# Performance work log

Measured on AMD Instinct MI355X. Metric: run time of the kernel, lower is better.

## Reference

```python
import jax, jax.numpy as jnp
import numpy as np

B, F, D = 32768, 2668, 64

def _xn(key, shape):
    # xavier_normal_: std = sqrt(2/(fan_in+fan_out))
    std = np.sqrt(2.0 / (shape[0] + shape[1]))
    return jax.random.normal(key, shape, dtype=jnp.float32) * std

def setup_inputs() -> dict:
    key = jax.random.key(0)
    ks = jax.random.split(key, 16)
    fv = jax.random.uniform(ks[0], (B, F), dtype=jnp.float32)
    sizes = [(1, 'age_user_w'), (1, 'age_item_w'), (2, 'gender_user_w'), (2, 'gender_item_w'),
             (21, 'occupation_user_w'), (21, 'occupation_item_w'), (19, 'movie_user_w'), (19, 'movie_item_w'),
             (943, 'userid_user_w'), (943, 'userid_item_w'), (1682, 'itemid_user_w'), (1682, 'itemid_item_w')]
    inp = {'feature_vector': fv}
    for i, (n, name) in enumerate(sizes):
        inp[name] = _xn(ks[i + 1], (n, D))
    # nn.Linear(F,1): kaiming-uniform weight, uniform bias; plain uniform scale suffices for a reference
    bound = 1.0 / np.sqrt(F)
    inp['lin_w'] = jax.random.uniform(ks[13], (1, F), dtype=jnp.float32, minval=-bound, maxval=bound)
    inp['lin_b'] = jax.random.uniform(ks[14], (1,), dtype=jnp.float32, minval=-bound, maxval=bound)
    return inp

def reference(feature_vector, age_user_w, age_item_w, gender_user_w, gender_item_w,
              occupation_user_w, occupation_item_w, movie_user_w, movie_item_w,
              userid_user_w, userid_item_w, itemid_user_w, itemid_item_w, lin_w, lin_b):
    fv = feature_vector
    au = fv[:, 2626:2627] @ age_user_w          # [B, D] (note: column 2626 reused, as in source)
    ai = fv[:, 2626:2627] @ age_item_w
    gu = fv[:, 2626:2628] @ gender_user_w
    gi = fv[:, 2626:2628] @ gender_item_w
    ou = fv[:, 2628:2649] @ occupation_user_w
    oi = fv[:, 2628:2649] @ occupation_item_w
    mu = fv[:, 2649:2668] @ movie_user_w
    mi = fv[:, 2649:2668] @ movie_item_w
    uu = fv[:, 0:943] @ userid_user_w
    ui = fv[:, 0:943] @ userid_item_w
    tu = fv[:, 943:2625] @ itemid_user_w
    ti = fv[:, 943:2625] @ itemid_item_w
    cross = jnp.sum(au * gu + au * ou + ai * mu + au * uu + ai * tu
                    + gu * ou + gi * mu + gu * uu + gi * tu
                    + oi * mu + ou * uu + oi * tu
                    + mu * ui + mi * ti + ui * tu, axis=1)   # [B]
    logits = fv @ lin_w.T + lin_b + cross[:, None]           # [B, 1]
    return jax.nn.sigmoid(logits)
```

## Files before the change

kernel.cpp:

```cpp
#include <hip/hip_runtime.h>

#define FDIM 2668

typedef float f32x4 __attribute__((ext_vector_type(4)));
typedef _Float16 f16x8 __attribute__((ext_vector_type(8)));

#define G1_NK 30
#define G2_NK 53
#define G3_NK 2
#define G1_NT 9
#define G2_NT 9
#define G3_NT 29
#define BUF_BYTES (G3_NT * 1024)

#define HU 0
#define HT (G1_NK * G1_NT * 512)
#define HS (HT + G2_NK * G2_NT * 512)
#define H_TOTAL (HS + G3_NK * G3_NT * 512)

__global__ __launch_bounds__(256) void ffm_prep(
    const float* __restrict__ au_, const float* __restrict__ ai_,
    const float* __restrict__ gu_, const float* __restrict__ gi_,
    const float* __restrict__ ou_, const float* __restrict__ oi_,
    const float* __restrict__ mu_, const float* __restrict__ mi_,
    const float* __restrict__ uu_, const float* __restrict__ ui_,
    const float* __restrict__ tu_, const float* __restrict__ ti_,
    const float* __restrict__ lw, _Float16* __restrict__ ws) {
  int e = blockIdx.x * 256 + threadIdx.x;
  if (e >= H_TOTAL) return;
  float val = 0.f;
  int rel, ntiles;
  if (e < HT) { rel = e; ntiles = G1_NT; }
  else if (e < HS) { rel = e - HT; ntiles = G2_NT; }
  else { rel = e - HS; ntiles = G3_NT; }
  int perk = ntiles * 512;
  int kb = rel / perk;
  int r = rel - kb * perk;
  int nt = r >> 9; r &= 511;
  int lane = r >> 3, j = r & 7;
  int k = kb * 32 + ((lane >> 4) << 3) + j;
  int n = (nt << 4) + (lane & 15);

  if (e < HT) {
    if (k < 943) {
      if (n < 64) val = uu_[k * 64 + n];
      else if (n < 128) val = ui_[k * 64 + n - 64];
      else if (n == 128) val = lw[k];
    }
  } else if (e < HS) {
    int col = 940 + k;
    if (n < 64) { if (col >= 943 && col < 2625) val = tu_[(col - 943) * 64 + n]; }
    else if (n < 128) { if (col >= 943 && col < 2625) val = ti_[(col - 943) * 64 + n - 64]; }
    else if (n == 128) { if (col >= 943 && col <= 2635) val = lw[col]; }
  } else {
    int col = 2624 + k;
    if (n == 448) { if (col >= 2636 && col < 2668) val = lw[col]; }
    else if (n < 448) {
      int blk = n >> 6, d = n & 63;
      float ageu = (col == 2626) ? au_[d] : 0.f;
      float agei = (col == 2626) ? ai_[d] : 0.f;
      float genu = (col >= 2626 && col < 2628) ? gu_[(col - 2626) * 64 + d] : 0.f;
      float geni = (col >= 2626 && col < 2628) ? gi_[(col - 2626) * 64 + d] : 0.f;
      float occu = (col >= 2628 && col < 2649) ? ou_[(col - 2628) * 64 + d] : 0.f;
      float occi = (col >= 2628 && col < 2649) ? oi_[(col - 2628) * 64 + d] : 0.f;
      float movu = (col >= 2649 && col < 2668) ? mu_[(col - 2649) * 64 + d] : 0.f;
      float movi = (col >= 2649 && col < 2668) ? mi_[(col - 2649) * 64 + d] : 0.f;
      switch (blk) {
        case 0: val = ageu + genu + occu; break;
        case 1: val = agei + geni + occi; break;
        case 2: val = movu; break;
        case 3: val = movi; break;
        case 4: val = ageu; break;
        case 5: val = genu; break;
        case 6: val = occu; break;
      }
    }
  }
  ws[e] = (_Float16)val;
}

template <int NT>
__device__ __forceinline__ void stageB(const _Float16* __restrict__ src, char* lds,
                                       int bufOff, int tid, int wave) {
  constexpr int chunks = NT * 64;
#pragma unroll
  for (int base = 0; base < chunks; base += 256) {
    int idx = base + tid;
    if (idx < chunks) {
      __builtin_amdgcn_global_load_lds(
          (const __attribute__((address_space(1))) void*)(src + (size_t)idx * 8),
          (__attribute__((address_space(3))) void*)(lds + bufOff + (base + wave * 64) * 16),
          16, 0, 0);
    }
  }
}

template <bool GUARD>
__device__ __forceinline__ void loadA(f32x4& a0, f32x4& a1,
                                      const float* __restrict__ myrow, int c0) {
  f32x4 z = {0.f, 0.f, 0.f, 0.f};
  if (!GUARD || (c0 + 4) <= FDIM) a0 = *(const f32x4*)(myrow + c0); else a0 = z;
  if (!GUARD || (c0 + 8) <= FDIM) a1 = *(const f32x4*)(myrow + c0 + 4); else a1 = z;
}

template <int NT, bool GUARD>
__device__ __forceinline__ void gemm_phase(const float* __restrict__ myrow, int colbase,
                                           int nk, const _Float16* __restrict__ wsrc,
                                           char* lds, int tid, int lane, int kg, int wave,
                                           f32x4* acc) {
  stageB<NT>(wsrc, lds, 0, tid, wave);
  f32x4 a0, a1;
  loadA<GUARD>(a0, a1, myrow, colbase + kg * 8);
  int cur = 0;
  for (int kb = 0; kb < nk; ++kb) {
    __syncthreads();
    f32x4 n0 = {0.f, 0.f, 0.f, 0.f}, n1 = {0.f, 0.f, 0.f, 0.f};
    if (kb + 1 < nk) {
      stageB<NT>(wsrc + (size_t)(kb + 1) * (NT * 512), lds, (cur ^ 1) * BUF_BYTES, tid, wave);
      loadA<GUARD>(n0, n1, myrow, colbase + (kb + 1) * 32 + kg * 8);
    }
    f16x8 af;
#pragma unroll
    for (int i = 0; i < 4; ++i) { af[i] = (_Float16)a0[i]; af[4 + i] = (_Float16)a1[i]; }
    const char* buf = lds + cur * BUF_BYTES + lane * 16;
#pragma unroll
    for (int nt = 0; nt < NT; ++nt) {
      f16x8 bf = *(const f16x8*)(buf + nt * 1024);
      acc[nt] = __builtin_amdgcn_mfma_f32_16x16x32_f16(af, bf, acc[nt], 0, 0, 0);
    }
    a0 = n0; a1 = n1;
    cur ^= 1;
  }
}

__global__ __launch_bounds__(256, 2) void ffm_main(
    const float* __restrict__ fv, const _Float16* __restrict__ wp,
    const float* __restrict__ linb, float* __restrict__ out) {
  __shared__ __align__(16) char lds[2 * BUF_BYTES];
  const int tid = threadIdx.x;
  const int lane = tid & 63;
  const int wave = tid >> 6;
  const int nl = lane & 15;
  const int kg = lane >> 4;
  const int rowbase = blockIdx.x * 64 + wave * 16;
  const float* myrow = fv + (size_t)(rowbase + nl) * FDIM;
  const f32x4 zero4 = {0.f, 0.f, 0.f, 0.f};

  f32x4 s[G3_NT];
#pragma unroll
  for (int i = 0; i < G3_NT; ++i) s[i] = zero4;
  gemm_phase<G3_NT, true>(myrow, 2624, G3_NK, wp + HS, lds, tid, lane, kg, wave, s);

  f32x4 P[4], Q[4], MU[4], MI[4];
  f32x4 cross = s[28];
#pragma unroll
  for (int t = 0; t < 4; ++t) {
    P[t] = s[t]; Q[t] = s[4 + t]; MU[t] = s[8 + t]; MI[t] = s[12 + t];
    cross += s[16 + t] * (s[20 + t] + s[24 + t]) + s[20 + t] * s[24 + t] + MU[t] * Q[t];
  }

  f32x4 u[G1_NT];
#pragma unroll
  for (int i = 0; i < G1_NT; ++i) u[i] = zero4;
  gemm_phase<G1_NT, false>(myrow, 0, G1_NK, wp + HU, lds, tid, lane, kg, wave, u);
  cross += u[8];
#pragma unroll
  for (int t = 0; t < 4; ++t) {
    cross += u[t] * P[t] + u[4 + t] * MU[t];
    Q[t] += u[4 + t];
  }

  f32x4 v[G2_NT];
#pragma unroll
  for (int i = 0; i < G2_NT; ++i) v[i] = zero4;
  gemm_phase<G2_NT, false>(myrow, 940, G2_NK, wp + HT, lds, tid, lane, kg, wave, v);
  cross += v[8];
#pragma unroll
  for (int t = 0; t < 4; ++t) {
    cross += v[t] * Q[t] + v[4 + t] * MI[t];
  }

  float c0 = cross[0], c1 = cross[1], c2 = cross[2], c3 = cross[3];
#pragma unroll
  for (int m = 1; m <= 8; m <<= 1) {
    c0 += __shfl_xor(c0, m, 64);
    c1 += __shfl_xor(c1, m, 64);
    c2 += __shfl_xor(c2, m, 64);
    c3 += __shfl_xor(c3, m, 64);
  }
  if (nl == 0) {
    float lb = linb[0];
    int r = rowbase + kg * 4;
    out[r + 0] = 1.f / (1.f + __expf(-(c0 + lb)));
    out[r + 1] = 1.f / (1.f + __expf(-(c1 + lb)));
    out[r + 2] = 1.f / (1.f + __expf(-(c2 + lb)));
    out[r + 3] = 1.f / (1.f + __expf(-(c3 + lb)));
  }
}

extern "C" void kernel_launch(void* const* d_in, const int* in_sizes, int n_in,
                              void* d_out, int out_size, void* d_ws, size_t ws_size,
                              hipStream_t stream) {
  const float* fv    = (const float*)d_in[0];
  const float* age_u = (const float*)d_in[1];
  const float* age_i = (const float*)d_in[2];
  const float* gen_u = (const float*)d_in[3];
  const float* gen_i = (const float*)d_in[4];
  const float* occ_u = (const float*)d_in[5];
  const float* occ_i = (const float*)d_in[6];
  const float* mov_u = (const float*)d_in[7];
  const float* mov_i = (const float*)d_in[8];
  const float* uid_u = (const float*)d_in[9];
  const float* uid_i = (const float*)d_in[10];
  const float* iid_u = (const float*)d_in[11];
  const float* iid_i = (const float*)d_in[12];
  const float* lin_w = (const float*)d_in[13];
  const float* lin_b = (const float*)d_in[14];
  _Float16* ws = (_Float16*)d_ws;
  float* out = (float*)d_out;

  ffm_prep<<<(H_TOTAL + 255) / 256, 256, 0, stream>>>(
      age_u, age_i, gen_u, gen_i, occ_u, occ_i, mov_u, mov_i,
      uid_u, uid_i, iid_u, iid_i, lin_w, ws);
  ffm_main<<<32768 / 64, 256, 0, stream>>>(fv, ws, lin_b, out);
}
```

Baseline: 505.0 us.

## Load packed B fragments directly from global memory, dropping LDS staging and barriers

```diff
diff --git a/kernel.cpp b/kernel.cpp
--- a/kernel.cpp
+++ b/kernel.cpp
@@ -4,6 +4,7 @@
 
 typedef float f32x4 __attribute__((ext_vector_type(4)));
 typedef _Float16 f16x8 __attribute__((ext_vector_type(8)));
+typedef __fp16 fp16x2 __attribute__((ext_vector_type(2)));
 
 #define G1_NK 30
 #define G2_NK 53
@@ -11,7 +12,6 @@
 #define G1_NT 9
 #define G2_NT 9
 #define G3_NT 29
-#define BUF_BYTES (G3_NT * 1024)
 
 #define HU 0
 #define HT (G1_NK * G1_NT * 512)
@@ -79,22 +79,6 @@
   ws[e] = (_Float16)val;
 }
 
-template <int NT>
-__device__ __forceinline__ void stageB(const _Float16* __restrict__ src, char* lds,
-                                       int bufOff, int tid, int wave) {
-  constexpr int chunks = NT * 64;
-#pragma unroll
-  for (int base = 0; base < chunks; base += 256) {
-    int idx = base + tid;
-    if (idx < chunks) {
-      __builtin_amdgcn_global_load_lds(
-          (const __attribute__((address_space(1))) void*)(src + (size_t)idx * 8),
-          (__attribute__((address_space(3))) void*)(lds + bufOff + (base + wave * 64) * 16),
-          16, 0, 0);
-    }
-  }
-}
-
 template <bool GUARD>
 __device__ __forceinline__ void loadA(f32x4& a0, f32x4& a1,
                                       const float* __restrict__ myrow, int c0) {
@@ -103,40 +87,38 @@
   if (!GUARD || (c0 + 8) <= FDIM) a1 = *(const f32x4*)(myrow + c0 + 4); else a1 = z;
 }
 
+__device__ __forceinline__ f16x8 cvtA(const f32x4& a0, const f32x4& a1) {
+  union { f16x8 v; fp16x2 h[4]; } u;
+  u.h[0] = __builtin_amdgcn_cvt_pkrtz(a0[0], a0[1]);
+  u.h[1] = __builtin_amdgcn_cvt_pkrtz(a0[2], a0[3]);
+  u.h[2] = __builtin_amdgcn_cvt_pkrtz(a1[0], a1[1]);
+  u.h[3] = __builtin_amdgcn_cvt_pkrtz(a1[2], a1[3]);
+  return u.v;
+}
+
 template <int NT, bool GUARD>
 __device__ __forceinline__ void gemm_phase(const float* __restrict__ myrow, int colbase,
                                            int nk, const _Float16* __restrict__ wsrc,
-                                           char* lds, int tid, int lane, int kg, int wave,
-                                           f32x4* acc) {
-  stageB<NT>(wsrc, lds, 0, tid, wave);
+                                           int lane, int kg, f32x4* acc) {
+  const _Float16* bptr = wsrc + (size_t)lane * 8;
   f32x4 a0, a1;
   loadA<GUARD>(a0, a1, myrow, colbase + kg * 8);
-  int cur = 0;
   for (int kb = 0; kb < nk; ++kb) {
-    __syncthreads();
     f32x4 n0 = {0.f, 0.f, 0.f, 0.f}, n1 = {0.f, 0.f, 0.f, 0.f};
-    if (kb + 1 < nk) {
-      stageB<NT>(wsrc + (size_t)(kb + 1) * (NT * 512), lds, (cur ^ 1) * BUF_BYTES, tid, wave);
-      loadA<GUARD>(n0, n1, myrow, colbase + (kb + 1) * 32 + kg * 8);
-    }
-    f16x8 af;
-#pragma unroll
-    for (int i = 0; i < 4; ++i) { af[i] = (_Float16)a0[i]; af[4 + i] = (_Float16)a1[i]; }
-    const char* buf = lds + cur * BUF_BYTES + lane * 16;
+    if (kb + 1 < nk) loadA<GUARD>(n0, n1, myrow, colbase + (kb + 1) * 32 + kg * 8);
+    f16x8 af = cvtA(a0, a1);
 #pragma unroll
     for (int nt = 0; nt < NT; ++nt) {
-      f16x8 bf = *(const f16x8*)(buf + nt * 1024);
+      f16x8 bf = *(const f16x8*)(bptr + (size_t)(kb * NT + nt) * 512);
       acc[nt] = __builtin_amdgcn_mfma_f32_16x16x32_f16(af, bf, acc[nt], 0, 0, 0);
     }
     a0 = n0; a1 = n1;
-    cur ^= 1;
   }
 }
 
 __global__ __launch_bounds__(256, 2) void ffm_main(
     const float* __restrict__ fv, const _Float16* __restrict__ wp,
     const float* __restrict__ linb, float* __restrict__ out) {
-  __shared__ __align__(16) char lds[2 * BUF_BYTES];
   const int tid = threadIdx.x;
   const int lane = tid & 63;
   const int wave = tid >> 6;
@@ -149,7 +131,7 @@
   f32x4 s[G3_NT];
 #pragma unroll
   for (int i = 0; i < G3_NT; ++i) s[i] = zero4;
-  gemm_phase<G3_NT, true>(myrow, 2624, G3_NK, wp + HS, lds, tid, lane, kg, wave, s);
+  gemm_phase<G3_NT, true>(myrow, 2624, G3_NK, wp + HS, lane, kg, s);
 
   f32x4 P[4], Q[4], MU[4], MI[4];
   f32x4 cross = s[28];
@@ -162,7 +144,7 @@
   f32x4 u[G1_NT];
 #pragma unroll
   for (int i = 0; i < G1_NT; ++i) u[i] = zero4;
-  gemm_phase<G1_NT, false>(myrow, 0, G1_NK, wp + HU, lds, tid, lane, kg, wave, u);
+  gemm_phase<G1_NT, false>(myrow, 0, G1_NK, wp + HU, lane, kg, u);
   cross += u[8];
 #pragma unroll
   for (int t = 0; t < 4; ++t) {
@@ -173,7 +155,7 @@
   f32x4 v[G2_NT];
 #pragma unroll
   for (int i = 0; i < G2_NT; ++i) v[i] = zero4;
-  gemm_phase<G2_NT, false>(myrow, 940, G2_NK, wp + HT, lds, tid, lane, kg, wave, v);
+  gemm_phase<G2_NT, false>(myrow, 940, G2_NK, wp + HT, lane, kg, v);
   cross += v[8];
 #pragma unroll
   for (int t = 0; t < 4; ++t) {
@@ -190,11 +172,12 @@
   }
   if (nl == 0) {
     float lb = linb[0];
-    int r = rowbase + kg * 4;
-    out[r + 0] = 1.f / (1.f + __expf(-(c0 + lb)));
-    out[r + 1] = 1.f / (1.f + __expf(-(c1 + lb)));
-    out[r + 2] = 1.f / (1.f + __expf(-(c2 + lb)));
-    out[r + 3] = 1.f / (1.f + __expf(-(c3 + lb)));
+    f32x4 o;
+    o[0] = 1.f / (1.f + __expf(-(c0 + lb)));
+    o[1] = 1.f / (1.f + __expf(-(c1 + lb)));
+    o[2] = 1.f / (1.f + __expf(-(c2 + lb)));
+    o[3] = 1.f / (1.f + __expf(-(c3 + lb)));
+    *(f32x4*)(out + rowbase + kg * 4) = o;
   }
 }
 
```

Result: slower. 541.2 us (+7.2%).
